# Optimization experiments

Hardware: AMD Instinct MI355X
Metric: run time of the kernel (lower is better)

## Reference

```python
import jax, jax.numpy as jnp
import numpy as np

B, C, H, W = 4, 256, 224, 224
WH = WW = 8
SH = SW = 4
HEADS = 8
HD = C // HEADS
N = WH * WW
EPS = 1e-5


def _rel_index():
    coords = np.stack(np.meshgrid(np.arange(WH), np.arange(WW), indexing='ij')).reshape(2, -1)
    rel = (coords[:, :, None] - coords[:, None, :]).transpose(1, 2, 0).copy()
    rel[:, :, 0] += WH - 1
    rel[:, :, 1] += WW - 1
    rel[:, :, 0] *= 2 * WW - 1
    return rel.sum(-1)  # (N, N) int

REL_INDEX = _rel_index()


def _shift_mask(Hp, Wp):
    # Swin shift mask for one image: (nW, N, N) float, 0 or -100
    img = np.zeros((Hp, Wp))
    cnt = 0
    for a, b in [(0, Hp - WH), (Hp - WH, Hp - SH), (Hp - SH, Hp)]:
        for c, d in [(0, Wp - WW), (Wp - WW, Wp - SW), (Wp - SW, Wp)]:
            img[a:b, c:d] = cnt
            cnt += 1
    mw = img.reshape(Hp // WH, WH, Wp // WW, WW).transpose(0, 2, 1, 3).reshape(-1, N)
    diff = mw[:, None, :] - mw[:, :, None]  # [w, i, j] = mw[w,j] - mw[w,i]
    return np.where(diff != 0, np.float32(-100.0), np.float32(0.0)).astype(np.float32)


def _ln(x, w, b):
    m = jnp.mean(x, axis=-1, keepdims=True)
    v = jnp.mean(jnp.square(x - m), axis=-1, keepdims=True)
    return (x - m) * jax.lax.rsqrt(v + EPS) * w + b


def setup_inputs() -> dict:
    key = jax.random.key(0)
    ks = jax.random.split(key, 8)
    num_rel = (2 * WH - 1) * (2 * WW - 1)
    return {
        'x': jax.random.normal(ks[0], (B, C, H, W), dtype=jnp.float32),
        'qkv_w': jax.random.normal(ks[1], (3 * C, C), dtype=jnp.float32) * 0.02,
        'proj_w': jax.random.normal(ks[2], (C, C), dtype=jnp.float32) * 0.02,
        'proj_b': jnp.zeros((C,), dtype=jnp.float32),
        'rpb_table': jax.random.normal(ks[3], (num_rel, HEADS), dtype=jnp.float32) * 0.02,
        'norm1_w': jnp.ones((C,), dtype=jnp.float32),
        'norm1_b': jnp.zeros((C,), dtype=jnp.float32),
        'norm2_w': jnp.ones((C,), dtype=jnp.float32),
        'norm2_b': jnp.zeros((C,), dtype=jnp.float32),
        'mlp_w1': jax.random.normal(ks[4], (4 * C, C), dtype=jnp.float32) * 0.02,
        'mlp_b1': jnp.zeros((4 * C,), dtype=jnp.float32),
        'mlp_w2': jax.random.normal(ks[5], (C, 4 * C), dtype=jnp.float32) * 0.02,
        'mlp_b2': jnp.zeros((C,), dtype=jnp.float32),
    }


def reference(x, qkv_w, proj_w, proj_b, rpb_table, norm1_w, norm1_b,
              norm2_w, norm2_b, mlp_w1, mlp_b1, mlp_w2, mlp_b2):
    Bx, Cx, Hx, Wx = x.shape
    pad_h = (WH - Hx % WH) % WH
    pad_w = (WW - Wx % WW) % WW
    if pad_h or pad_w:
        x = jnp.pad(x, ((0, 0), (0, 0), (0, pad_h), (0, pad_w)))
    Hp, Wp = Hx + pad_h, Wx + pad_w
    x = jnp.transpose(x, (0, 2, 3, 1))                    # BHWC
    x = jnp.roll(x, (-SH, -SW), axis=(1, 2))
    nW = (Hp // WH) * (Wp // WW)
    # window partition -> (B*nW, N, C), batch-major
    xw = x.reshape(Bx, Hp // WH, WH, Wp // WW, WW, Cx)
    xw = jnp.transpose(xw, (0, 1, 3, 2, 4, 5)).reshape(-1, N, Cx)

    # ----- windowed attention -----
    h = _ln(xw, norm1_w, norm1_b)
    qkv = (h @ qkv_w.T).reshape(-1, N, 3, HEADS, HD)
    qkv = jnp.transpose(qkv, (2, 0, 3, 1, 4))             # (3, Bw, heads, N, hd)
    q, k, v = qkv[0], qkv[1], qkv[2]
    attn = jnp.einsum('bhnd,bhmd->bhnm', q, k) * (1.0 / HD ** 0.5)
    bias = jnp.transpose(rpb_table[REL_INDEX.reshape(-1)].reshape(N, N, HEADS), (2, 0, 1))
    attn = attn + bias[None]
    # faithful to torch: repeat_interleave(B, dim=0) -> window-major mask ordering
    mask = jnp.asarray(_shift_mask(Hp, Wp))               # (nW, N, N)
    attn = attn + jnp.repeat(mask, Bx, axis=0)[:, None]
    attn = jax.nn.softmax(attn, axis=-1)
    out = jnp.einsum('bhnm,bhmd->bhnd', attn, v)
    out = jnp.transpose(out, (0, 2, 1, 3)).reshape(-1, N, Cx)
    out = out @ proj_w.T + proj_b
    xw = xw + out

    # ----- MLP -----
    h = _ln(xw, norm2_w, norm2_b)
    h = jax.nn.gelu(h @ mlp_w1.T + mlp_b1, approximate=False) @ mlp_w2.T + mlp_b2
    xw = xw + h

    # window reverse, un-shift, un-pad
    x = xw.reshape(Bx, Hp // WH, Wp // WW, WH, WW, Cx)
    x = jnp.transpose(x, (0, 1, 3, 2, 4, 5)).reshape(Bx, Hp, Wp, Cx)
    x = jnp.roll(x, (SH, SW), axis=(1, 2))
    x = x[:, :Hx, :Wx, :]
    return jnp.transpose(x, (0, 3, 1, 2))
```

## Files before the change

kernel.cpp:

```cpp
#include <hip/hip_runtime.h>

typedef unsigned short u16;
typedef unsigned int   u32;
typedef __attribute__((ext_vector_type(8))) __bf16 bf16x8;
typedef __attribute__((ext_vector_type(4))) float  f32x4;
typedef __attribute__((ext_vector_type(4))) u16    u16x4;
typedef __attribute__((ext_vector_type(8))) u16    u16x8;

#define DEV __device__ __forceinline__

DEV u16 f2b(float f) {
  union { float f; u32 u; } a; a.f = f;
  const u32 u = a.u;
  return (u16)((u + 0x7fffu + ((u >> 16) & 1u)) >> 16);
}

DEV float gelu_fast(float x) {
  const float x2 = x * x;
  const float t  = __builtin_fmaf(0.1029430f, x2, 2.3022150f);
  const float e  = __builtin_exp2f(x * t);
  const float r  = __builtin_amdgcn_rcpf(1.0f + e);
  return __builtin_fmaf(-x, r, x);
}

DEV void gload16(const void* g, void* l) {
  __builtin_amdgcn_global_load_lds(
      (const __attribute__((address_space(1))) void*)g,
      (__attribute__((address_space(3))) void*)l, 16, 0, 0);
}

__global__ __launch_bounds__(256)
void conv_weights(const float* __restrict__ qkvw, const float* __restrict__ projw,
                  const float* __restrict__ w1,   const float* __restrict__ w2,
                  u16* __restrict__ dq, u16* __restrict__ dp,
                  u16* __restrict__ d1, u16* __restrict__ d2) {
  const int t = blockIdx.x * 256 + threadIdx.x;
  if (t < 196608)      dq[t]          = f2b(qkvw[t]);
  else if (t < 262144) dp[t - 196608] = f2b(projw[t - 196608]);
  else if (t < 524288) d1[t - 262144] = f2b(w1[t - 262144]);
  else                 d2[t - 524288] = f2b(w2[t - 524288]);
}

__global__ __launch_bounds__(256)
void ln1_win(const float* __restrict__ x, const float* __restrict__ w1,
             const float* __restrict__ b1, u16* __restrict__ hout,
             float* __restrict__ xwout) {
  __shared__ float xt[64 * 257];
  __shared__ float smean[256], srstd[256];
  const int tid = threadIdx.x, lane = tid & 63, wv = tid >> 6;
  const int g = blockIdx.x;
  const int b = g / 196, rem = g % 196;
  const int wh = rem / 7, wg = rem % 7;
  const int base_r = b * 784 + wh * 28 + wg * 4;
  const int pr = tid >> 5, pc = tid & 31;
  int hp = wh * 8 + 4 + pr; if (hp >= 224) hp -= 224;
  int wp = wg * 32 + 4 + pc; if (wp >= 224) wp -= 224;
  const long roff = (long)b * 256 * 50176 + hp * 224 + wp;

  float s = 0.f, q = 0.f;
  for (int cc = 0; cc < 4; ++cc) {
#pragma unroll 8
    for (int i = 0; i < 64; ++i) {
      const int c = cc * 64 + i;
      const float v = x[(long)c * 50176 + roff];
      xt[i * 257 + tid] = v;
      s += v; q += v * v;
    }
    __syncthreads();
#pragma unroll 8
    for (int jj = 0; jj < 64; ++jj) {
      const int p = jj * 4 + wv;
      const int m = (base_r + ((p & 31) >> 3)) * 64 + (p >> 5) * 8 + (p & 7);
      xwout[(long)m * 256 + cc * 64 + lane] = xt[lane * 257 + p];
    }
    __syncthreads();
  }
  const float mean = s * (1.f / 256.f);
  smean[tid] = mean;
  srstd[tid] = rsqrtf(q * (1.f / 256.f) - mean * mean + 1e-5f);
  __syncthreads();

  float wr_[4], br_[4];
#pragma unroll
  for (int cc = 0; cc < 4; ++cc) { wr_[cc] = w1[cc * 64 + lane]; br_[cc] = b1[cc * 64 + lane]; }
#pragma unroll 2
  for (int jj = 0; jj < 64; ++jj) {
    const int p = jj * 4 + wv;
    const int m = (base_r + ((p & 31) >> 3)) * 64 + (p >> 5) * 8 + (p & 7);
    const float mu = smean[p], rs = srstd[p];
#pragma unroll
    for (int cc = 0; cc < 4; ++cc) {
      const float v = xwout[(long)m * 256 + cc * 64 + lane];
      hout[(long)m * 256 + cc * 64 + lane] = f2b((v - mu) * rs * wr_[cc] + br_[cc]);
    }
  }
}

template<int EPI, int NCOL>
__global__ __launch_bounds__(512, 4)
void gemm_bt(const u16* __restrict__ A, const u16* __restrict__ Bw, const int K,
             float* __restrict__ fout, const float* __restrict__ bias,
             u16* __restrict__ bout,
             const float* __restrict__ lnw, const float* __restrict__ lnb,
             float* __restrict__ oout) {
  __shared__ __align__(16) u16 smem[36864];

  const int tid  = threadIdx.x;
  const int lane = tid & 63;
  const int wid  = tid >> 6;
  const int wrr  = wid >> 2;
  const int wcc  = wid & 3;

  const int nwg = gridDim.x;
  const int bid = blockIdx.x;
  const int wg  = (bid & 7) * (nwg >> 3) + (bid >> 3);
  const int row0 = wg * 128;

  const f32x4 vzero = {0.f, 0.f, 0.f, 0.f};

  const int l15  = lane & 15;
  const int l4   = lane >> 4;
  const int ksw2 = (l15 >> 1) & 3;
  const int lcol = (((tid & 3) ^ ((tid >> 3) & 3)) << 3);

  const u16* pA = A + (long)(row0 + (tid >> 2)) * K + lcol;
  const int wbase = wid * 512;

#define STAGE_TILE(KT, DA, DB)                  \
  {                                             \
    gload16(pA  + (KT), (DA) + wbase);          \
    gload16(pB  + (KT), (DB) + wbase);          \
    gload16(pB2 + (KT), (DB) + 4096 + wbase);   \
  }

#define COMPUTE_TILE(SA, SB, SWAP)                                                      \
  {                                                                                     \
    bf16x8 af[4], bfv[4];                                                               \
    _Pragma("unroll")                                                                   \
    for (int mi = 0; mi < 4; ++mi)                                                      \
      af[mi] = *(const bf16x8*)((SA) + (wrr * 64 + mi * 16 + l15) * 32 +                \
                                ((l4 ^ ksw2) << 3));                                    \
    _Pragma("unroll")                                                                   \
    for (int nj = 0; nj < 4; ++nj)                                                      \
      bfv[nj] = *(const bf16x8*)((SB) + (wcc * 64 + nj * 16 + l15) * 32 +               \
                                 ((l4 ^ ksw2) << 3));                                   \
    _Pragma("unroll")                                                                   \
    for (int mi = 0; mi < 4; ++mi)                                                      \
      _Pragma("unroll")                                                                 \
      for (int nj = 0; nj < 4; ++nj) {                                                  \
        if (SWAP)                                                                       \
          acc[mi][nj] = __builtin_amdgcn_mfma_f32_16x16x32_bf16(bfv[nj], af[mi],        \
                                                                acc[mi][nj], 0, 0, 0);  \
        else                                                                            \
          acc[mi][nj] = __builtin_amdgcn_mfma_f32_16x16x32_bf16(af[mi], bfv[nj],        \
                                                                acc[mi][nj], 0, 0, 0);  \
      }                                                                                 \
  }

#define KLOOP(SWAP)                                                  \
  {                                                                  \
    const int nt = K >> 5;                                           \
    u16 *A0 = smem,          *B0 = smem + 4096;                      \
    u16 *A1 = smem + 12288,  *B1 = smem + 16384;                     \
    u16 *A2 = smem + 24576,  *B2 = smem + 28672;                     \
    STAGE_TILE(0, A0, B0);                                           \
    STAGE_TILE(32, A1, B1);                                          \
    for (int t = 0; t < nt; ++t) {                                   \
      if (t + 2 < nt) {                                              \
        STAGE_TILE((t + 2) << 5, A2, B2);                            \
        asm volatile("s_waitcnt vmcnt(6)" ::: "memory");             \
      } else if (t + 1 < nt) {                                       \
        asm volatile("s_waitcnt vmcnt(3)" ::: "memory");             \
      } else {                                                       \
        asm volatile("s_waitcnt vmcnt(0)" ::: "memory");             \
      }                                                              \
      __builtin_amdgcn_s_barrier();                                  \
      asm volatile("" ::: "memory");                                 \
      COMPUTE_TILE(A0, B0, SWAP);                                    \
      asm volatile("" ::: "memory");                                 \
      __builtin_amdgcn_s_barrier();                                  \
      u16* tA = A0; A0 = A1; A1 = A2; A2 = tA;                       \
      u16* tB = B0; B0 = B1; B1 = B2; B2 = tB;                       \
    }                                                                \
  }

#pragma unroll
  for (int cb = 0; cb < NCOL; ++cb) {
    const int col0 = cb * 256;
    const u16* pB  = Bw + (long)(col0 + (tid >> 2)) * K + lcol;
    const u16* pB2 = pB + (long)128 * K;

    f32x4 acc[4][4];
#pragma unroll
    for (int i = 0; i < 4; ++i)
#pragma unroll
      for (int j = 0; j < 4; ++j) acc[i][j] = vzero;

    if (EPI == 0 && cb == 2) {
      KLOOP(0);
#pragma unroll
      for (int mi = 0; mi < 4; ++mi) {
        const int mb = row0 + wrr * 64 + mi * 16 + (l4 << 2);
        const int rrg = mb >> 6, ii = mb & 63;
#pragma unroll
        for (int nj = 0; nj < 4; ++nj) {
          const int n = 512 + wcc * 64 + nj * 16 + l15;
          const int hh = (n >> 5) & 7, d = n & 31;
          u16x4 p;
#pragma unroll
          for (int reg = 0; reg < 4; ++reg) p[reg] = f2b(acc[mi][nj][reg]);
          *(u16x4*)(bout + 102760448L + (long)((rrg * 8 + hh) * 32 + d) * 64 + ii) = p;
        }
      }
      continue;
    }

    KLOOP(1);

    if (EPI == 0) {
#pragma unroll
      for (int mi = 0; mi < 4; ++mi) {
        const int m = row0 + wrr * 64 + mi * 16 + l15;
        const int rr = m >> 6, ii = m & 63;
#pragma unroll
        for (int nj = 0; nj < 4; ++nj) {
          const int n = col0 + wcc * 64 + nj * 16 + (l4 << 2);
          const int s = n >> 8, hh = (n >> 5) & 7, d = n & 31;
          u16x4 p;
#pragma unroll
          for (int reg = 0; reg < 4; ++reg) p[reg] = f2b(acc[mi][nj][reg]);
          *(u16x4*)(bout + (long)s * 51380224L +
                    (long)((rr * 8 + hh) * 64 + ii) * 32 + d) = p;
        }
      }
    } else if (EPI == 1) {
      f32x4 b4[4];
#pragma unroll
      for (int nj = 0; nj < 4; ++nj)
        b4[nj] = *(const f32x4*)(bias + wcc * 64 + nj * 16 + (l4 << 2));
      float sS[4], sQ[4];
#pragma unroll
      for (int mi = 0; mi < 4; ++mi) {
        const int m = row0 + wrr * 64 + mi * 16 + l15;
        float* yrow = fout + (long)m * 256;
        float s = 0.f, q = 0.f;
#pragma unroll
        for (int nj = 0; nj < 4; ++nj) {
          const int n = wcc * 64 + nj * 16 + (l4 << 2);
          f32x4 o = *(f32x4*)(yrow + n);
#pragma unroll
          for (int reg = 0; reg < 4; ++reg) {
            o[reg] += acc[mi][nj][reg] + b4[nj][reg];
            s += o[reg]; q += o[reg] * o[reg];
          }
          *(f32x4*)(yrow + n) = o;
          acc[mi][nj] = o;
        }
        s += __shfl_xor(s, 16); s += __shfl_xor(s, 32);
        q += __shfl_xor(q, 16); q += __shfl_xor(q, 32);
        sS[mi] = s; sQ[mi] = q;
      }
      float* ps = (float*)smem;
      float* pq = ps + 512;
      __syncthreads();
      if (lane < 16) {
#pragma unroll
        for (int mi = 0; mi < 4; ++mi) {
          const int idx = (wrr * 64 + mi * 16 + l15) * 4 + wcc;
          ps[idx] = sS[mi]; pq[idx] = sQ[mi];
        }
      }
      __syncthreads();
#pragma unroll
      for (int mi = 0; mi < 4; ++mi) {
        const int m = row0 + wrr * 64 + mi * 16 + l15;
        const int base = (wrr * 64 + mi * 16 + l15) * 4;
        const float S = ps[base] + ps[base + 1] + ps[base + 2] + ps[base + 3];
        const float Q = pq[base] + pq[base + 1] + pq[base + 2] + pq[base + 3];
        const float mean = S * (1.f / 256.f);
        const float rstd = rsqrtf(Q * (1.f / 256.f) - mean * mean + 1e-5f);
#pragma unroll
        for (int nj = 0; nj < 4; ++nj) {
          const int n = wcc * 64 + nj * 16 + (l4 << 2);
          const f32x4 w4 = *(const f32x4*)(lnw + n);
          const f32x4 c4 = *(const f32x4*)(lnb + n);
          u16x4 p;
#pragma unroll
          for (int reg = 0; reg < 4; ++reg)
            p[reg] = f2b((acc[mi][nj][reg] - mean) * rstd * w4[reg] + c4[reg]);
          *(u16x4*)(bout + (long)m * 256 + n) = p;
        }
      }
    } else if (EPI == 3) {
      f32x4 b4[4];
#pragma unroll
      for (int nj = 0; nj < 4; ++nj)
        b4[nj] = *(const f32x4*)(bias + wcc * 64 + nj * 16 + (l4 << 2));
#pragma unroll
      for (int mi = 0; mi < 4; ++mi) {
        const int m = row0 + wrr * 64 + mi * 16 + l15;
        const float* yrow = fout + (long)m * 256;
#pragma unroll
        for (int nj = 0; nj < 4; ++nj) {
          const int n = wcc * 64 + nj * 16 + (l4 << 2);
          const f32x4 yv = *(const f32x4*)(yrow + n);
#pragma unroll
          for (int reg = 0; reg < 4; ++reg)
            acc[mi][nj][reg] += yv[reg] + b4[nj][reg];
        }
      }
      const int wr0 = row0 >> 6;
      const int b = wr0 / 784, rem = wr0 % 784;
      const int wh = rem / 28, wwb = rem % 28;
      float* tp = (float*)smem;
      const int pidx = tid & 127, cgrp = tid >> 7;
      const int pr = pidx >> 4, pc = pidx & 15;
      int hp = wh * 8 + 4 + pr;  if (hp >= 224) hp -= 224;
      int wp = wwb * 8 + 4 + pc; if (wp >= 224) wp -= 224;
      float* ob = oout + (long)b * 256 * 50176 + hp * 224 + wp;
#pragma unroll
      for (int cc = 0; cc < 4; ++cc) {
        __syncthreads();
        if (wcc == cc) {
#pragma unroll
          for (int mi = 0; mi < 4; ++mi) {
            const int ml = wrr * 64 + mi * 16 + l15;
            const int px = ((ml & 63) >> 3) * 16 + (ml >> 6) * 8 + (ml & 7);
#pragma unroll
            for (int nj = 0; nj < 4; ++nj)
#pragma unroll
              for (int reg = 0; reg < 4; ++reg)
                tp[(nj * 16 + (l4 << 2) + reg) * 128 + (px ^ (l4 << 2))] =
                    acc[mi][nj][reg];
          }
        }
        __syncthreads();
#pragma unroll 4
        for (int j = 0; j < 16; ++j) {
          const int cl = cgrp * 16 + j;
          ob[(long)(cc * 64 + cl) * 50176] =
              tp[cl * 128 + (pidx ^ (((cl >> 2) & 3) << 2))];
        }
      }
    } else if (EPI == 2) {
      f32x4 b4[4];
#pragma unroll
      for (int nj = 0; nj < 4; ++nj)
        b4[nj] = *(const f32x4*)(bias + col0 + wcc * 64 + nj * 16 + (l4 << 2));
#pragma unroll
      for (int mi = 0; mi < 4; ++mi) {
        const int m = row0 + wrr * 64 + mi * 16 + l15;
#pragma unroll
        for (int nj = 0; nj < 4; ++nj) {
          const int n = col0 + wcc * 64 + nj * 16 + (l4 << 2);
          u16x4 p;
#pragma unroll
          for (int reg = 0; reg < 4; ++reg)
            p[reg] = f2b(gelu_fast(acc[mi][nj][reg] + b4[nj][reg]));
          *(u16x4*)(bout + (long)m * 1024 + n) = p;
        }
      }
    }
  }

#undef STAGE_TILE
#undef COMPUTE_TILE
#undef KLOOP
}

__global__ __launch_bounds__(256)
void attn_win(const u16* __restrict__ qkv, const float* __restrict__ rpb,
              u16* __restrict__ aout) {
  __shared__ u16 Pl[4][4096];
  __shared__ float srpb[1800];
  const int tid = threadIdx.x, lane = tid & 63, wv = tid >> 6;
  const int bid = blockIdx.x;
  const int r = bid >> 1;
  const int h = (bid & 1) * 4 + wv;
  for (int i = tid; i < 1800; i += 256) srpb[i] = rpb[i];
  __syncthreads();

  const int midx = r >> 2;
  const int wh = midx / 28, ww = midx % 28;
  const int l15 = lane & 15, l4 = lane >> 4;

  u16* Pw = &Pl[wv][0];
  const long hb = (long)(r * 8 + h) * 2048;
  const u16* qh = qkv + hb;
  const u16* kh = qkv + 51380224 + hb;
  const u16* vh = qkv + 102760448 + hb;

  int rj[4], cj[4], labj[4];
#pragma unroll
  for (int nj = 0; nj < 4; ++nj) {
    const int j = nj * 16 + l15;
    rj[nj] = j >> 3; cj[nj] = j & 7;
    const int hp = wh * 8 + rj[nj], wp = ww * 8 + cj[nj];
    const int lh = (hp < 216) ? 0 : ((hp < 220) ? 1 : 2);
    const int lw = (wp < 216) ? 0 : ((wp < 220) ? 1 : 2);
    labj[nj] = lh * 3 + lw;
  }

  const f32x4 vzero = {0.f, 0.f, 0.f, 0.f};

  bf16x8 qf[4], kf[4];
#pragma unroll
  for (int mi = 0; mi < 4; ++mi)
    qf[mi] = *(const bf16x8*)(qh + (mi * 16 + l15) * 32 + l4 * 8);
#pragma unroll
  for (int nj = 0; nj < 4; ++nj)
    kf[nj] = *(const bf16x8*)(kh + (nj * 16 + l15) * 32 + l4 * 8);

  f32x4 S[4][4];
#pragma unroll
  for (int mi = 0; mi < 4; ++mi)
#pragma unroll
    for (int nj = 0; nj < 4; ++nj)
      S[mi][nj] = __builtin_amdgcn_mfma_f32_16x16x32_bf16(qf[mi], kf[nj], vzero, 0, 0, 0);

#pragma unroll
  for (int mi = 0; mi < 4; ++mi)
#pragma unroll
    for (int reg = 0; reg < 4; ++reg) {
      const int i = mi * 16 + (l4 << 2) + reg;
      const int ri = i >> 3, ci = i & 7;
      const int hp = wh * 8 + ri, wp = ww * 8 + ci;
      const int lh = (hp < 216) ? 0 : ((hp < 220) ? 1 : 2);
      const int lw = (wp < 216) ? 0 : ((wp < 220) ? 1 : 2);
      const int li = lh * 3 + lw;
      float v[4];
#pragma unroll
      for (int nj = 0; nj < 4; ++nj) {
        const int idx = (ri - rj[nj] + 7) * 15 + (ci - cj[nj] + 7);
        v[nj] = S[mi][nj][reg] * 0.17677669529663687f + srpb[idx * 8 + h]
              + ((li != labj[nj]) ? -100.0f : 0.0f);
      }
      float mx = fmaxf(fmaxf(v[0], v[1]), fmaxf(v[2], v[3]));
      mx = fmaxf(mx, __shfl_xor(mx, 1));
      mx = fmaxf(mx, __shfl_xor(mx, 2));
      mx = fmaxf(mx, __shfl_xor(mx, 4));
      mx = fmaxf(mx, __shfl_xor(mx, 8));
      float sum = 0.f;
#pragma unroll
      for (int nj = 0; nj < 4; ++nj) { v[nj] = __expf(v[nj] - mx); sum += v[nj]; }
      sum += __shfl_xor(sum, 1);
      sum += __shfl_xor(sum, 2);
      sum += __shfl_xor(sum, 4);
      sum += __shfl_xor(sum, 8);
      const float rinv = __builtin_amdgcn_rcpf(sum);
      const int sw = (i & 7) << 3;
#pragma unroll
      for (int nj = 0; nj < 4; ++nj)
        Pw[i * 64 + ((nj * 16 + l15) ^ sw)] = f2b(v[nj] * rinv);
    }

  f32x4 OT[2][4];
#pragma unroll
  for (int td = 0; td < 2; ++td)
#pragma unroll
    for (int ti = 0; ti < 4; ++ti) OT[td][ti] = vzero;

  const int rsw = (l15 & 7) << 3;
#pragma unroll
  for (int kk = 0; kk < 2; ++kk) {
    bf16x8 pf[4], vf[2];
#pragma unroll
    for (int ti = 0; ti < 4; ++ti)
      pf[ti] = *(const bf16x8*)(Pw + (ti * 16 + l15) * 64 + ((kk * 32 + l4 * 8) ^ rsw));
#pragma unroll
    for (int td = 0; td < 2; ++td)
      vf[td] = *(const bf16x8*)(vh + (td * 16 + l15) * 64 + kk * 32 + l4 * 8);
#pragma unroll
    for (int td = 0; td < 2; ++td)
#pragma unroll
      for (int ti = 0; ti < 4; ++ti)
        OT[td][ti] = __builtin_amdgcn_mfma_f32_16x16x32_bf16(vf[td], pf[ti], OT[td][ti], 0, 0, 0);
  }

#pragma unroll
  for (int td = 0; td < 2; ++td)
#pragma unroll
    for (int ti = 0; ti < 4; ++ti) {
      const int i = ti * 16 + l15;
      const int d0 = td * 16 + (l4 << 2);
      u16x4 p;
#pragma unroll
      for (int reg = 0; reg < 4; ++reg) p[reg] = f2b(OT[td][ti][reg]);
      *(u16x4*)(aout + (long)(r * 64 + i) * 256 + h * 32 + d0) = p;
    }
}

extern "C" void kernel_launch(void* const* d_in, const int* in_sizes, int n_in,
                              void* d_out, int out_size, void* d_ws, size_t ws_size,
                              hipStream_t stream) {
  (void)in_sizes; (void)n_in; (void)out_size; (void)ws_size;
  const float* x     = (const float*)d_in[0];
  const float* qkvw  = (const float*)d_in[1];
  const float* projw = (const float*)d_in[2];
  const float* projb = (const float*)d_in[3];
  const float* rpb   = (const float*)d_in[4];
  const float* n1w   = (const float*)d_in[5];
  const float* n1b   = (const float*)d_in[6];
  const float* n2w   = (const float*)d_in[7];
  const float* n2b   = (const float*)d_in[8];
  const float* w1    = (const float*)d_in[9];
  const float* b1    = (const float*)d_in[10];
  const float* w2    = (const float*)d_in[11];
  const float* b2    = (const float*)d_in[12];

  char* ws = (char*)d_ws;
  u16*   hbuf   = (u16*)(ws);
  u16*   qkvb   = (u16*)(ws + 102760448);
  u16*   abuf   = (u16*)(ws + 411041792);
  float* ybuf   = (float*)(ws + 513802240);
  u16*   hidb   = (u16*)(ws + 102760448);
  u16*   qkvwb  = (u16*)(ws + 719323136);
  u16*   projwb = (u16*)(ws + 719716352);
  u16*   w1b    = (u16*)(ws + 719847424);
  u16*   w2b    = (u16*)(ws + 720371712);

  conv_weights<<<3072, 256, 0, stream>>>(qkvw, projw, w1, w2, qkvwb, projwb, w1b, w2b);
  ln1_win<<<784, 256, 0, stream>>>(x, n1w, n1b, hbuf, ybuf);
  gemm_bt<0, 3><<<1568, 512, 0, stream>>>(hbuf, qkvwb, 256, nullptr, nullptr, qkvb, nullptr, nullptr, nullptr);
  attn_win<<<6272, 256, 0, stream>>>(qkvb, rpb, abuf);
  gemm_bt<1, 1><<<1568, 512, 0, stream>>>(abuf, projwb, 256, ybuf, projb, hbuf, n2w, n2b, nullptr);
  gemm_bt<2, 4><<<1568, 512, 0, stream>>>(hbuf, w1b, 256, nullptr, b1, hidb, nullptr, nullptr, nullptr);
  gemm_bt<3, 1><<<1568, 512, 0, stream>>>(hidb, w2b, 1024, ybuf, b2, nullptr, nullptr, nullptr, (float*)d_out);
}
```

Measured before the change: 1.155 ms.

## Enlarge GEMM tile to 256x256 with BK=64 double-buffered phased k-loop

The GEMM kernel's tile grows from 128x256 to 256x256 rows per workgroup with a K-step of 64, halving the grid and doubling the accumulators per wave. The triple-buffered 32-wide k-loop becomes a double-buffered loop split into four MFMA phases, with the next tile's global loads spread across those phases and MFMA priority raised via setprio. The aim is more operand reuse per LDS load and less barrier and load overhead per FLOP. In exchange it uses more registers and LDS, which cuts occupancy (launch bounds 4 to 2), and the epilogues are rescaled to the larger tile.

```diff
diff --git a/kernel.cpp b/kernel.cpp
--- a/kernel.cpp
+++ b/kernel.cpp
@@ -5,7 +5,6 @@
 typedef __attribute__((ext_vector_type(8))) __bf16 bf16x8;
 typedef __attribute__((ext_vector_type(4))) float  f32x4;
 typedef __attribute__((ext_vector_type(4))) u16    u16x4;
-typedef __attribute__((ext_vector_type(8))) u16    u16x8;
 
 #define DEV __device__ __forceinline__
 
@@ -97,13 +96,13 @@
 }
 
 template<int EPI, int NCOL>
-__global__ __launch_bounds__(512, 4)
+__global__ __launch_bounds__(512, 2)
 void gemm_bt(const u16* __restrict__ A, const u16* __restrict__ Bw, const int K,
              float* __restrict__ fout, const float* __restrict__ bias,
              u16* __restrict__ bout,
              const float* __restrict__ lnw, const float* __restrict__ lnb,
              float* __restrict__ oout) {
-  __shared__ __align__(16) u16 smem[36864];
+  __shared__ __align__(16) u16 smem[65536];
 
   const int tid  = threadIdx.x;
   const int lane = tid & 63;
@@ -114,93 +113,108 @@
   const int nwg = gridDim.x;
   const int bid = blockIdx.x;
   const int wg  = (bid & 7) * (nwg >> 3) + (bid >> 3);
-  const int row0 = wg * 128;
+  const int row0 = wg * 256;
 
   const f32x4 vzero = {0.f, 0.f, 0.f, 0.f};
 
   const int l15  = lane & 15;
   const int l4   = lane >> 4;
-  const int ksw2 = (l15 >> 1) & 3;
-  const int lcol = (((tid & 3) ^ ((tid >> 3) & 3)) << 3);
-
-  const u16* pA = A + (long)(row0 + (tid >> 2)) * K + lcol;
-  const int wbase = wid * 512;
-
-#define STAGE_TILE(KT, DA, DB)                  \
-  {                                             \
-    gload16(pA  + (KT), (DA) + wbase);          \
-    gload16(pB  + (KT), (DB) + wbase);          \
-    gload16(pB2 + (KT), (DB) + 4096 + wbase);   \
-  }
-
-#define COMPUTE_TILE(SA, SB, SWAP)                                                      \
+  const int ksw  = (l15 & 7) << 3;
+  const int srow = tid >> 3;
+  const int ksrc = (((tid & 7) ^ (srow & 7)) << 3);
+
+  const u16* pA = A + (long)(row0 + srow) * K + ksrc;
+
+#define STAGE_A(I, DST, KT) gload16(pA + (long)((I) * 64) * K + (KT), (DST) + (I) * 4096 + wid * 512)
+#define STAGE_B(I, DST, KT) gload16(pB + (long)((I) * 64) * K + (KT), (DST) + (I) * 4096 + wid * 512)
+
+#define RD_A(BUF, MI, KK) (*(const bf16x8*)((BUF) + (wrr * 128 + (MI) * 16 + l15) * 64 + \
+                                            (((KK) * 32 + l4 * 8) ^ ksw)))
+#define RD_B(BUF, NJ, KK) (*(const bf16x8*)((BUF) + (wcc * 64 + (NJ) * 16 + l15) * 64 + \
+                                            (((KK) * 32 + l4 * 8) ^ ksw)))
+
+#define PHASE_MM(CA, CB, MH, KK, LOADB, SWAP)                                           \
   {                                                                                     \
-    bf16x8 af[4], bfv[4];                                                               \
+    bf16x8 af_[4];                                                                      \
+    if (LOADB) {                                                                        \
+      _Pragma("unroll")                                                                 \
+      for (int nj = 0; nj < 4; ++nj) bfv[nj] = RD_B(CB, nj, KK);                        \
+    }                                                                                   \
     _Pragma("unroll")                                                                   \
-    for (int mi = 0; mi < 4; ++mi)                                                      \
-      af[mi] = *(const bf16x8*)((SA) + (wrr * 64 + mi * 16 + l15) * 32 +                \
-                                ((l4 ^ ksw2) << 3));                                    \
-    _Pragma("unroll")                                                                   \
-    for (int nj = 0; nj < 4; ++nj)                                                      \
-      bfv[nj] = *(const bf16x8*)((SB) + (wcc * 64 + nj * 16 + l15) * 32 +               \
-                                 ((l4 ^ ksw2) << 3));                                   \
+    for (int mi = 0; mi < 4; ++mi) af_[mi] = RD_A(CA, (MH) * 4 + mi, KK);               \
+    __builtin_amdgcn_s_setprio(1);                                                      \
     _Pragma("unroll")                                                                   \
     for (int mi = 0; mi < 4; ++mi)                                                      \
       _Pragma("unroll")                                                                 \
       for (int nj = 0; nj < 4; ++nj) {                                                  \
         if (SWAP)                                                                       \
-          acc[mi][nj] = __builtin_amdgcn_mfma_f32_16x16x32_bf16(bfv[nj], af[mi],        \
-                                                                acc[mi][nj], 0, 0, 0);  \
+          acc[(MH) * 4 + mi][nj] = __builtin_amdgcn_mfma_f32_16x16x32_bf16(             \
+              bfv[nj], af_[mi], acc[(MH) * 4 + mi][nj], 0, 0, 0);                       \
         else                                                                            \
-          acc[mi][nj] = __builtin_amdgcn_mfma_f32_16x16x32_bf16(af[mi], bfv[nj],        \
-                                                                acc[mi][nj], 0, 0, 0);  \
+          acc[(MH) * 4 + mi][nj] = __builtin_amdgcn_mfma_f32_16x16x32_bf16(             \
+              af_[mi], bfv[nj], acc[(MH) * 4 + mi][nj], 0, 0, 0);                       \
       }                                                                                 \
-  }
-
-#define KLOOP(SWAP)                                                  \
-  {                                                                  \
-    const int nt = K >> 5;                                           \
-    u16 *A0 = smem,          *B0 = smem + 4096;                      \
-    u16 *A1 = smem + 12288,  *B1 = smem + 16384;                     \
-    u16 *A2 = smem + 24576,  *B2 = smem + 28672;                     \
-    STAGE_TILE(0, A0, B0);                                           \
-    STAGE_TILE(32, A1, B1);                                          \
-    for (int t = 0; t < nt; ++t) {                                   \
-      if (t + 2 < nt) {                                              \
-        STAGE_TILE((t + 2) << 5, A2, B2);                            \
-        asm volatile("s_waitcnt vmcnt(6)" ::: "memory");             \
-      } else if (t + 1 < nt) {                                       \
-        asm volatile("s_waitcnt vmcnt(3)" ::: "memory");             \
-      } else {                                                       \
-        asm volatile("s_waitcnt vmcnt(0)" ::: "memory");             \
-      }                                                              \
-      __builtin_amdgcn_s_barrier();                                  \
-      asm volatile("" ::: "memory");                                 \
-      COMPUTE_TILE(A0, B0, SWAP);                                    \
-      asm volatile("" ::: "memory");                                 \
-      __builtin_amdgcn_s_barrier();                                  \
-      u16* tA = A0; A0 = A1; A1 = A2; A2 = tA;                       \
-      u16* tB = B0; B0 = B1; B1 = B2; B2 = tB;                       \
-    }                                                                \
+    __builtin_amdgcn_s_setprio(0);                                                      \
+  }
+
+#define FENCE asm volatile("" ::: "memory")
+#define BAR   __builtin_amdgcn_s_barrier()
+
+#define KLOOP(SWAP)                                                       \
+  {                                                                       \
+    const int nt = K >> 6;                                                \
+    u16 *A0 = smem,          *B0 = smem + 16384;                          \
+    u16 *A1 = smem + 32768,  *B1 = smem + 49152;                          \
+    _Pragma("unroll")                                                     \
+    for (int i = 0; i < 4; ++i) { STAGE_A(i, A0, 0); STAGE_B(i, B0, 0); } \
+    int cur = 0;                                                          \
+    for (int t = 0; t < nt; ++t) {                                        \
+      u16 *cA = cur ? A1 : A0, *cB = cur ? B1 : B0;                       \
+      u16 *nA = cur ? A0 : A1, *nB = cur ? B0 : B1;                       \
+      const int kt1 = (t + 1) << 6;                                       \
+      bf16x8 bfv[4];                                                      \
+                                                                 \
+      if (t + 1 < nt) {                                                   \
+        STAGE_A(0, nA, kt1); STAGE_A(1, nA, kt1);                         \
+        asm volatile("s_waitcnt vmcnt(2)" ::: "memory");                  \
+      } else {                                                            \
+        asm volatile("s_waitcnt vmcnt(0)" ::: "memory");                  \
+      }                                                                   \
+      BAR; FENCE;                                                         \
+      PHASE_MM(cA, cB, 0, 0, 1, SWAP);                                    \
+      FENCE; BAR;                                                         \
+                                                                 \
+      if (t + 1 < nt) { STAGE_A(2, nA, kt1); STAGE_A(3, nA, kt1); }       \
+      PHASE_MM(cA, cB, 1, 0, 0, SWAP);                                    \
+      FENCE; BAR;                                                         \
+                                                                 \
+      if (t + 1 < nt) { STAGE_B(0, nB, kt1); STAGE_B(1, nB, kt1); }       \
+      PHASE_MM(cA, cB, 0, 1, 1, SWAP);                                    \
+      FENCE; BAR;                                                         \
+                                                                 \
+      if (t + 1 < nt) { STAGE_B(2, nB, kt1); STAGE_B(3, nB, kt1); }       \
+      PHASE_MM(cA, cB, 1, 1, 0, SWAP);                                    \
+      FENCE; BAR;                                                         \
+      cur ^= 1;                                                           \
+    }                                                                     \
   }
 
 #pragma unroll
   for (int cb = 0; cb < NCOL; ++cb) {
     const int col0 = cb * 256;
-    const u16* pB  = Bw + (long)(col0 + (tid >> 2)) * K + lcol;
-    const u16* pB2 = pB + (long)128 * K;
-
-    f32x4 acc[4][4];
-#pragma unroll
-    for (int i = 0; i < 4; ++i)
+    const u16* pB = Bw + (long)(col0 + srow) * K + ksrc;
+
+    f32x4 acc[8][4];
+#pragma unroll
+    for (int i = 0; i < 8; ++i)
 #pragma unroll
       for (int j = 0; j < 4; ++j) acc[i][j] = vzero;
 
     if (EPI == 0 && cb == 2) {
       KLOOP(0);
 #pragma unroll
-      for (int mi = 0; mi < 4; ++mi) {
-        const int mb = row0 + wrr * 64 + mi * 16 + (l4 << 2);
+      for (int mi = 0; mi < 8; ++mi) {
+        const int mb = row0 + wrr * 128 + mi * 16 + (l4 << 2);
         const int rrg = mb >> 6, ii = mb & 63;
 #pragma unroll
         for (int nj = 0; nj < 4; ++nj) {
@@ -219,8 +233,8 @@
 
     if (EPI == 0) {
 #pragma unroll
-      for (int mi = 0; mi < 4; ++mi) {
-        const int m = row0 + wrr * 64 + mi * 16 + l15;
+      for (int mi = 0; mi < 8; ++mi) {
+        const int m = row0 + wrr * 128 + mi * 16 + l15;
         const int rr = m >> 6, ii = m & 63;
 #pragma unroll
         for (int nj = 0; nj < 4; ++nj) {
@@ -238,10 +252,10 @@
 #pragma unroll
       for (int nj = 0; nj < 4; ++nj)
         b4[nj] = *(const f32x4*)(bias + wcc * 64 + nj * 16 + (l4 << 2));
-      float sS[4], sQ[4];
-#pragma unroll
-      for (int mi = 0; mi < 4; ++mi) {
-        const int m = row0 + wrr * 64 + mi * 16 + l15;
+      float sS[8], sQ[8];
+#pragma unroll
+      for (int mi = 0; mi < 8; ++mi) {
+        const int m = row0 + wrr * 128 + mi * 16 + l15;
         float* yrow = fout + (long)m * 256;
         float s = 0.f, q = 0.f;
 #pragma unroll
@@ -261,20 +275,20 @@
         sS[mi] = s; sQ[mi] = q;
       }
       float* ps = (float*)smem;
-      float* pq = ps + 512;
+      float* pq = ps + 1024;
       __syncthreads();
       if (lane < 16) {
 #pragma unroll
-        for (int mi = 0; mi < 4; ++mi) {
-          const int idx = (wrr * 64 + mi * 16 + l15) * 4 + wcc;
+        for (int mi = 0; mi < 8; ++mi) {
+          const int idx = (wrr * 128 + mi * 16 + l15) * 4 + wcc;
           ps[idx] = sS[mi]; pq[idx] = sQ[mi];
         }
       }
       __syncthreads();
 #pragma unroll
-      for (int mi = 0; mi < 4; ++mi) {
-        const int m = row0 + wrr * 64 + mi * 16 + l15;
-        const int base = (wrr * 64 + mi * 16 + l15) * 4;
+      for (int mi = 0; mi < 8; ++mi) {
+        const int m = row0 + wrr * 128 + mi * 16 + l15;
+        const int base = (wrr * 128 + mi * 16 + l15) * 4;
         const float S = ps[base] + ps[base + 1] + ps[base + 2] + ps[base + 3];
         const float Q = pq[base] + pq[base + 1] + pq[base + 2] + pq[base + 3];
         const float mean = S * (1.f / 256.f);
@@ -297,8 +311,8 @@
       for (int nj = 0; nj < 4; ++nj)
         b4[nj] = *(const f32x4*)(bias + wcc * 64 + nj * 16 + (l4 << 2));
 #pragma unroll
-      for (int mi = 0; mi < 4; ++mi) {
-        const int m = row0 + wrr * 64 + mi * 16 + l15;
+      for (int mi = 0; mi < 8; ++mi) {
+        const int m = row0 + wrr * 128 + mi * 16 + l15;
         const float* yrow = fout + (long)m * 256;
 #pragma unroll
         for (int nj = 0; nj < 4; ++nj) {
@@ -313,8 +327,8 @@
       const int b = wr0 / 784, rem = wr0 % 784;
       const int wh = rem / 28, wwb = rem % 28;
       float* tp = (float*)smem;
-      const int pidx = tid & 127, cgrp = tid >> 7;
-      const int pr = pidx >> 4, pc = pidx & 15;
+      const int pidx = tid & 255, cgrp = tid >> 8;
+      const int pr = pidx >> 5, pc = pidx & 31;
       int hp = wh * 8 + 4 + pr;  if (hp >= 224) hp -= 224;
       int wp = wwb * 8 + 4 + pc; if (wp >= 224) wp -= 224;
       float* ob = oout + (long)b * 256 * 50176 + hp * 224 + wp;
@@ -323,23 +337,24 @@
         __syncthreads();
         if (wcc == cc) {
 #pragma unroll
-          for (int mi = 0; mi < 4; ++mi) {
-            const int ml = wrr * 64 + mi * 16 + l15;
-            const int px = ((ml & 63) >> 3) * 16 + (ml >> 6) * 8 + (ml & 7);
+          for (int mi = 0; mi < 8; ++mi) {
+            const int ml = wrr * 128 + mi * 16 + l15;
+            const int inner = ml & 63;
+            const int px = (inner >> 3) * 32 + (ml >> 6) * 8 + (inner & 7);
 #pragma unroll
             for (int nj = 0; nj < 4; ++nj)
 #pragma unroll
               for (int reg = 0; reg < 4; ++reg)
-                tp[(nj * 16 + (l4 << 2) + reg) * 128 + (px ^ (l4 << 2))] =
+                tp[(nj * 16 + (l4 << 2) + reg) * 256 + (px ^ (l4 << 3))] =
                     acc[mi][nj][reg];
           }
         }
         __syncthreads();
 #pragma unroll 4
-        for (int j = 0; j < 16; ++j) {
-          const int cl = cgrp * 16 + j;
+        for (int j = 0; j < 32; ++j) {
+          const int cl = cgrp * 32 + j;
           ob[(long)(cc * 64 + cl) * 50176] =
-              tp[cl * 128 + (pidx ^ (((cl >> 2) & 3) << 2))];
+              tp[cl * 256 + (pidx ^ (((cl >> 2) & 3) << 3))];
         }
       }
     } else if (EPI == 2) {
@@ -348,8 +363,8 @@
       for (int nj = 0; nj < 4; ++nj)
         b4[nj] = *(const f32x4*)(bias + col0 + wcc * 64 + nj * 16 + (l4 << 2));
 #pragma unroll
-      for (int mi = 0; mi < 4; ++mi) {
-        const int m = row0 + wrr * 64 + mi * 16 + l15;
+      for (int mi = 0; mi < 8; ++mi) {
+        const int m = row0 + wrr * 128 + mi * 16 + l15;
 #pragma unroll
         for (int nj = 0; nj < 4; ++nj) {
           const int n = col0 + wcc * 64 + nj * 16 + (l4 << 2);
@@ -363,8 +378,13 @@
     }
   }
 
-#undef STAGE_TILE
-#undef COMPUTE_TILE
+#undef STAGE_A
+#undef STAGE_B
+#undef RD_A
+#undef RD_B
+#undef PHASE_MM
+#undef FENCE
+#undef BAR
 #undef KLOOP
 }
 
@@ -521,9 +541,9 @@
 
   conv_weights<<<3072, 256, 0, stream>>>(qkvw, projw, w1, w2, qkvwb, projwb, w1b, w2b);
   ln1_win<<<784, 256, 0, stream>>>(x, n1w, n1b, hbuf, ybuf);
-  gemm_bt<0, 3><<<1568, 512, 0, stream>>>(hbuf, qkvwb, 256, nullptr, nullptr, qkvb, nullptr, nullptr, nullptr);
+  gemm_bt<0, 3><<<784, 512, 0, stream>>>(hbuf, qkvwb, 256, nullptr, nullptr, qkvb, nullptr, nullptr, nullptr);
   attn_win<<<6272, 256, 0, stream>>>(qkvb, rpb, abuf);
-  gemm_bt<1, 1><<<1568, 512, 0, stream>>>(abuf, projwb, 256, ybuf, projb, hbuf, n2w, n2b, nullptr);
-  gemm_bt<2, 4><<<1568, 512, 0, stream>>>(hbuf, w1b, 256, nullptr, b1, hidb, nullptr, nullptr, nullptr);
-  gemm_bt<3, 1><<<1568, 512, 0, stream>>>(hidb, w2b, 1024, ybuf, b2, nullptr, nullptr, nullptr, (float*)d_out);
-}
+  gemm_bt<1, 1><<<784, 512, 0, stream>>>(abuf, projwb, 256, ybuf, projb, hbuf, n2w, n2b, nullptr);
+  gemm_bt<2, 4><<<784, 512, 0, stream>>>(hbuf, w1b, 256, nullptr, b1, hidb, nullptr, nullptr, nullptr);
+  gemm_bt<3, 1><<<784, 512, 0, stream>>>(hidb, w2b, 1024, ybuf, b2, nullptr, nullptr, nullptr, (float*)d_out);
+}
```

New measurement: 1.172 ms. About the same (+1.5%).
